# Kernel optimization log

Hardware: AMD Instinct MI355X
Metric: run time of the kernel (lower is better)

The kernel has to match this reference:

```python
import jax, jax.numpy as jnp
import numpy as np

N = 100000          # nodes
DEG = 32            # fixed in-degree (every node has a non-empty mailbox)
E = N * DEG         # edges
IN_DIM = 25         # node feature dim; 3 aggregators * 1 scaler * 25 = 75
OUT_DIM = 128
AGG_EPS = 1e-5      # PNA std aggregator epsilon
BN_EPS = 1e-5       # BatchNorm1d epsilon


def setup_inputs() -> dict:
    key = jax.random.key(0)
    k = jax.random.split(key, 6)
    h = jax.random.normal(k[0], (N, IN_DIM), dtype=jnp.float32)
    snorm_n = jax.random.uniform(k[1], (N, 1), dtype=jnp.float32)
    # every node appears exactly DEG times as a destination -> degree 32
    edge_dst = jnp.repeat(jnp.arange(N, dtype=jnp.int32), DEG)
    edge_src = jax.random.randint(k[2], (E,), 0, N, dtype=jnp.int32)
    # posttrans MLP (1 layer): Linear(75 -> 128), no final activation
    W = jax.random.normal(k[3], (3 * IN_DIM, OUT_DIM), dtype=jnp.float32) / np.sqrt(3 * IN_DIM)
    b = jnp.zeros((OUT_DIM,), dtype=jnp.float32)
    # BatchNorm1d affine params
    gamma = jnp.ones((OUT_DIM,), dtype=jnp.float32)
    beta = jnp.zeros((OUT_DIM,), dtype=jnp.float32)
    return {"h": h, "snorm_n": snorm_n, "edge_src": edge_src, "edge_dst": edge_dst,
            "W": W, "b": b, "gamma": gamma, "beta": beta}


def reference(h, snorm_n, edge_src, edge_dst, W, b, gamma, beta):
    # --- message: e = src node features (pretrans_edges + message_func) ---
    e = h[edge_src]                                   # [E, IN_DIM] irregular gather
    # --- reduce: mean / max / std over each destination's mailbox ---
    ones = jnp.ones((e.shape[0],), dtype=h.dtype)
    deg = jax.ops.segment_sum(ones, edge_dst, num_segments=N)
    deg = jnp.maximum(deg, 1.0)[:, None]              # [N, 1]
    s1 = jax.ops.segment_sum(e, edge_dst, num_segments=N)
    mean = s1 / deg                                   # aggregate_mean
    mx = jax.ops.segment_max(e, edge_dst, num_segments=N)  # aggregate_max
    s2 = jax.ops.segment_sum(e * e, edge_dst, num_segments=N)
    var = jax.nn.relu(s2 / deg - mean * mean)         # aggregate_var
    std = jnp.sqrt(var + AGG_EPS)                     # aggregate_std
    agg = jnp.concatenate([mean, mx, std], axis=1)    # [N, 75]; identity scaler only
    # --- posttrans MLP: single Linear(75 -> 128), last_activation='none' ---
    z = agg @ W + b                                   # [N, OUT_DIM]
    # --- graph norm ---
    z = z * snorm_n
    # --- BatchNorm1d (training mode: batch statistics, biased variance) ---
    mu = jnp.mean(z, axis=0)
    v = jnp.var(z, axis=0)
    z = (z - mu) / jnp.sqrt(v + BN_EPS) * gamma + beta
    # --- relu; residual disabled (in_dim != out_dim); dropout p=0.0 is no-op ---
    return jax.nn.relu(z)
```

## Files before the change

### kernel.cpp

```cpp
#include <hip/hip_runtime.h>
#include <hip/hip_bf16.h>

#define NN 100000
#define DEG 32
#define IN_DIM 25
#define AGG_DIM 75
#define KPAD 104
#define OUT_DIM 128
#define NPB 16
#define EPC (NPB * DEG)
#define NCHUNK (NN / NPB)
#define BLK 256
#define GRID 2048
#define PREP_GRID 391

typedef __attribute__((ext_vector_type(8))) short short8;
typedef __attribute__((ext_vector_type(4))) float f32x4;

static __device__ __forceinline__ unsigned f2bf(float x) {
    __hip_bfloat16 h = __float2bfloat16(x);
    return (unsigned)*reinterpret_cast<unsigned short*>(&h);
}
static __device__ __forceinline__ float bflo(unsigned v) { return __uint_as_float(v << 16); }
static __device__ __forceinline__ float bfhi(unsigned v) { return __uint_as_float(v & 0xffff0000u); }

static __device__ __forceinline__ void gload16(const void* g, void* l) {
    __builtin_amdgcn_global_load_lds(
        (const __attribute__((address_space(1))) unsigned*)g,
        (__attribute__((address_space(3))) unsigned*)l, 16, 0, 0);
}

__global__ __launch_bounds__(BLK) void prep(const float* __restrict__ h,
                                            ushort* __restrict__ hbp,
                                            float* __restrict__ bnbuf) {
    const int t = threadIdx.x;
    const int gid = blockIdx.x * BLK + t;
    if (gid < 2 * OUT_DIM) bnbuf[gid] = 0.0f;
    for (int n = gid; n < NN; n += PREP_GRID * BLK) {
        const float* row = h + n * IN_DIM;
        unsigned u[16];
        #pragma unroll
        for (int k = 0; k < 12; ++k) u[k] = f2bf(row[2 * k]) | (f2bf(row[2 * k + 1]) << 16);
        u[12] = f2bf(row[24]);
        u[13] = 0u; u[14] = 0u; u[15] = 0u;
        uint4* dst = (uint4*)(hbp + (size_t)n * 32);
        dst[0] = make_uint4(u[0], u[1], u[2], u[3]);
        dst[1] = make_uint4(u[4], u[5], u[6], u[7]);
        dst[2] = make_uint4(u[8], u[9], u[10], u[11]);
        dst[3] = make_uint4(u[12], u[13], u[14], u[15]);
    }
}

__global__ __launch_bounds__(BLK) void pna_main(
    const ushort* __restrict__ hb, const float* __restrict__ snorm,
    const int* __restrict__ esrc, const float* __restrict__ W,
    const float* __restrict__ b, float* __restrict__ z,
    float* __restrict__ bnbuf)
{
    __shared__ __align__(1024) ushort E_s[EPC][32];
    __shared__ int    ids_s[EPC];
    __shared__ ushort agg[NPB][KPAD];

    const int t = threadIdx.x;
    const int lane = t & 63;
    const int wv = t >> 6;

    for (int i = t; i < NPB * KPAD; i += BLK) ((ushort*)agg)[i] = 0;

    const int cb0 = (wv * 2 + 0) * 16 + (lane & 15);
    const int cb1 = (wv * 2 + 1) * 16 + (lane & 15);
    short8 bfrag[2][3];
    #pragma unroll
    for (int ct = 0; ct < 2; ++ct) {
        const int cb = ct ? cb1 : cb0;
        #pragma unroll
        for (int kt = 0; kt < 3; ++kt) {
            short8 fr;
            #pragma unroll
            for (int j = 0; j < 8; ++j) {
                const int k = kt * 32 + ((lane >> 4) * 8) + j;
                const float w = (k < AGG_DIM) ? W[k * OUT_DIM + cb] : 0.0f;
                fr[j] = (short)f2bf(w);
            }
            bfrag[ct][kt] = fr;
        }
    }
    const float bb0 = b[cb0], bb1 = b[cb1];

    const int lsub = lane >> 2;
    const int prt  = lane & 3;
    const int nl2 = t >> 4;
    const int f2  = t & 15;
    const bool a2act = (f2 < 13);
    const int dcol = f2 ^ ((nl2 & 3) << 2);

    float bns0 = 0.f, bnq0 = 0.f, bns1 = 0.f, bnq1 = 0.f;

    for (int chunk = blockIdx.x; chunk < NCHUNK; chunk += GRID) {
        const int n0 = chunk * NPB;

        ((int2*)ids_s)[t] = ((const int2*)(esrc + n0 * DEG))[t];
        __syncthreads();

        #pragma unroll
        for (int i = 0; i < 8; ++i) {
            const int g = wv * 8 + i;
            const int r = g * 16 + lsub;
            const int src = ids_s[r];
            const int psrc = prt ^ ((r >> 5) & 3);
            gload16((const char*)hb + ((size_t)src << 6) + (psrc << 4),
                    (char*)E_s + (g << 10));
        }
        __syncthreads();

        if (a2act) {
            const unsigned* Ew = (const unsigned*)E_s;
            const unsigned base = (unsigned)(nl2 * 512 + dcol);
            float s0 = 0.f, q0 = 0.f, m0 = -3.4e38f;
            float s1 = 0.f, q1 = 0.f, m1 = -3.4e38f;
            #pragma unroll
            for (int e = 0; e < 32; ++e) {
                const int ee = (e + nl2) & 31;
                const unsigned v = Ew[base + ee * 16];
                const float lo = bflo(v), hi = bfhi(v);
                s0 += lo; q0 = fmaf(lo, lo, q0); m0 = fmaxf(m0, lo);
                s1 += hi; q1 = fmaf(hi, hi, q1); m1 = fmaxf(m1, hi);
            }
            const float inv = 1.0f / DEG;
            const float mean0 = s0 * inv, var0 = fmaxf(q0 * inv - mean0 * mean0, 0.f);
            const float mean1 = s1 * inv, var1 = fmaxf(q1 * inv - mean1 * mean1, 0.f);
            const int ff = f2 * 2;
            agg[nl2][ff]              = (ushort)f2bf(mean0);
            agg[nl2][IN_DIM + ff]     = (ushort)f2bf(m0);
            agg[nl2][2 * IN_DIM + ff] = (ushort)f2bf(sqrtf(var0 + 1e-5f));
            if (ff + 1 < IN_DIM) {
                agg[nl2][ff + 1]              = (ushort)f2bf(mean1);
                agg[nl2][IN_DIM + ff + 1]     = (ushort)f2bf(m1);
                agg[nl2][2 * IN_DIM + ff + 1] = (ushort)f2bf(sqrtf(var1 + 1e-5f));
            }
        }
        __syncthreads();

        const int arow = lane & 15;
        const int ak0  = (lane >> 4) * 8;
        f32x4 acc0 = {0.f, 0.f, 0.f, 0.f}, acc1 = {0.f, 0.f, 0.f, 0.f};
        #pragma unroll
        for (int kt = 0; kt < 3; ++kt) {
            const short8 af = *reinterpret_cast<const short8*>(&agg[arow][kt * 32 + ak0]);
            acc0 = __builtin_amdgcn_mfma_f32_16x16x32_bf16(af, bfrag[0][kt], acc0, 0, 0, 0);
            acc1 = __builtin_amdgcn_mfma_f32_16x16x32_bf16(af, bfrag[1][kt], acc1, 0, 0, 0);
        }
        const int r0 = (lane >> 4) * 4;
        #pragma unroll
        for (int r = 0; r < 4; ++r) {
            const int node = n0 + r0 + r;
            const float sn = snorm[node];
            const float v0 = (acc0[r] + bb0) * sn;
            const float v1 = (acc1[r] + bb1) * sn;
            z[node * OUT_DIM + cb0] = v0;
            z[node * OUT_DIM + cb1] = v1;
            bns0 += v0; bnq0 = fmaf(v0, v0, bnq0);
            bns1 += v1; bnq1 = fmaf(v1, v1, bnq1);
        }
    }

    bns0 += __shfl_xor(bns0, 16); bnq0 += __shfl_xor(bnq0, 16);
    bns0 += __shfl_xor(bns0, 32); bnq0 += __shfl_xor(bnq0, 32);
    bns1 += __shfl_xor(bns1, 16); bnq1 += __shfl_xor(bnq1, 16);
    bns1 += __shfl_xor(bns1, 32); bnq1 += __shfl_xor(bnq1, 32);
    if ((lane >> 4) == 0) {
        atomicAdd(&bnbuf[cb0], bns0);
        atomicAdd(&bnbuf[OUT_DIM + cb0], bnq0);
        atomicAdd(&bnbuf[cb1], bns1);
        atomicAdd(&bnbuf[OUT_DIM + cb1], bnq1);
    }
}

__global__ __launch_bounds__(BLK) void bn_apply(
    const float* __restrict__ bnbuf, const float* __restrict__ gamma,
    const float* __restrict__ beta, float* __restrict__ z)
{
    __shared__ float sc_s[OUT_DIM], sh_s[OUT_DIM];
    const int t = threadIdx.x;
    if (t < OUT_DIM) {
        const float mu = bnbuf[t] * (1.0f / NN);
        const float v  = fmaxf(bnbuf[OUT_DIM + t] * (1.0f / NN) - mu * mu, 0.0f);
        const float sc = gamma[t] * rsqrtf(v + 1e-5f);
        sc_s[t] = sc;
        sh_s[t] = beta[t] - mu * sc;
    }
    __syncthreads();
    const int c4 = (t & 31) * 4;
    const float s0 = sc_s[c4], s1 = sc_s[c4+1], s2 = sc_s[c4+2], s3 = sc_s[c4+3];
    const float h0 = sh_s[c4], h1 = sh_s[c4+1], h2 = sh_s[c4+2], h3 = sh_s[c4+3];

    float4* z4 = (float4*)z;
    const int total4 = NN * (OUT_DIM / 4);
    for (int i = blockIdx.x * BLK + t; i < total4; i += gridDim.x * BLK) {
        float4 v = z4[i];
        v.x = fmaxf(fmaf(v.x, s0, h0), 0.f);
        v.y = fmaxf(fmaf(v.y, s1, h1), 0.f);
        v.z = fmaxf(fmaf(v.z, s2, h2), 0.f);
        v.w = fmaxf(fmaf(v.w, s3, h3), 0.f);
        z4[i] = v;
    }
}

extern "C" void kernel_launch(void* const* d_in, const int* in_sizes, int n_in,
                              void* d_out, int out_size, void* d_ws, size_t ws_size,
                              hipStream_t stream) {
    const float* h     = (const float*)d_in[0];
    const float* snorm = (const float*)d_in[1];
    const int*   esrc  = (const int*)d_in[2];
    const float* W     = (const float*)d_in[4];
    const float* b     = (const float*)d_in[5];
    const float* gamma = (const float*)d_in[6];
    const float* beta  = (const float*)d_in[7];
    float*  z     = (float*)d_out;
    float*  bnbuf = (float*)d_ws;
    ushort* hbp   = (ushort*)((char*)d_ws + 1024);

    prep<<<PREP_GRID, BLK, 0, stream>>>(h, hbp, bnbuf);
    pna_main<<<GRID, BLK, 0, stream>>>(hbp, snorm, esrc, W, b, z, bnbuf);
    bn_apply<<<2048, BLK, 0, stream>>>(bnbuf, gamma, beta, z);
}
```

Baseline: 186.2 us.

## Split gather into two feature-half passes staged in output buffer before matmul

The bf16 node table is split into two 32-byte halves (features 0-15 and 16-24), and the fused kernel is replaced by two gather/aggregate passes, one per half, plus a separate matmul kernel. Each pass writes its per-node aggregates into the output buffer as scratch, and the matmul kernel reads them back, reassembles the 75-wide row and applies the MFMA, snorm and BN statistics. The aim is to shrink each random gather's working set so the table fits better in cache, and to coalesce the prep kernel's reads through shared memory. The cost is two extra kernel launches, a second pass over the edge indices, and an extra global write and read of intermediate aggregates, which depends on the later z writes not overrunning slabs that have yet to be read.

```diff
diff --git a/kernel.cpp b/kernel.cpp
--- a/kernel.cpp
+++ b/kernel.cpp
@@ -5,14 +5,19 @@
 #define DEG 32
 #define IN_DIM 25
 #define AGG_DIM 75
+#define OUT_DIM 128
+#define BLK 256
+
+#define GNPB 32
+#define GEPC (GNPB * DEG)
+#define GGRID (NN / GNPB)
+
+#define MNPB 16
+#define MGRID 3125
 #define KPAD 104
-#define OUT_DIM 128
-#define NPB 16
-#define EPC (NPB * DEG)
-#define NCHUNK (NN / NPB)
-#define BLK 256
-#define GRID 2048
-#define PREP_GRID 391
+
+#define PREP_NPB 128
+#define PREP_GRID ((NN + PREP_NPB - 1) / PREP_NPB)
 
 typedef __attribute__((ext_vector_type(8))) short short8;
 typedef __attribute__((ext_vector_type(4))) float f32x4;
@@ -23,52 +28,128 @@
 }
 static __device__ __forceinline__ float bflo(unsigned v) { return __uint_as_float(v << 16); }
 static __device__ __forceinline__ float bfhi(unsigned v) { return __uint_as_float(v & 0xffff0000u); }
-
 static __device__ __forceinline__ void gload16(const void* g, void* l) {
     __builtin_amdgcn_global_load_lds(
         (const __attribute__((address_space(1))) unsigned*)g,
         (__attribute__((address_space(3))) unsigned*)l, 16, 0, 0);
 }
 
+
 __global__ __launch_bounds__(BLK) void prep(const float* __restrict__ h,
-                                            ushort* __restrict__ hbp,
+                                            ushort* __restrict__ tabA,
+                                            ushort* __restrict__ tabB,
                                             float* __restrict__ bnbuf) {
+    __shared__ float hls[PREP_NPB * IN_DIM];
+    const int t = threadIdx.x, bk = blockIdx.x;
+    if (bk == 0 && t < 2 * OUT_DIM) bnbuf[t] = 0.0f;
+    const int base4 = bk * (PREP_NPB * IN_DIM / 4);
+    const float4* h4 = (const float4*)h;
+    for (int i = t; i < PREP_NPB * IN_DIM / 4; i += BLK)
+        if (base4 + i < NN * IN_DIM / 4) ((float4*)hls)[i] = h4[base4 + i];
+    __syncthreads();
+    const int nl = t >> 1, sel = t & 1;
+    const int node = bk * PREP_NPB + nl;
+    if (node < NN) {
+        const float* row = hls + nl * IN_DIM;
+        unsigned u[8];
+        if (sel == 0) {
+            #pragma unroll
+            for (int k = 0; k < 8; ++k) u[k] = f2bf(row[2*k]) | (f2bf(row[2*k+1]) << 16);
+            uint4* d = (uint4*)(tabA + (size_t)node * 16);
+            d[0] = make_uint4(u[0],u[1],u[2],u[3]);
+            d[1] = make_uint4(u[4],u[5],u[6],u[7]);
+        } else {
+            #pragma unroll
+            for (int k = 0; k < 4; ++k) u[k] = f2bf(row[16+2*k]) | (f2bf(row[17+2*k]) << 16);
+            u[4] = f2bf(row[24]); u[5] = 0u; u[6] = 0u; u[7] = 0u;
+            uint4* d = (uint4*)(tabB + (size_t)node * 16);
+            d[0] = make_uint4(u[0],u[1],u[2],u[3]);
+            d[1] = make_uint4(u[4],u[5],u[6],u[7]);
+        }
+    }
+}
+
+template<int NF, int ODW, int OOFF>
+__global__ __launch_bounds__(BLK) void gather_pass(
+    const ushort* __restrict__ tab, const int* __restrict__ esrc,
+    unsigned* __restrict__ zdw)
+{
+    __shared__ __align__(1024) unsigned E_s[GEPC * 8];
+    __shared__ int ids_s[GEPC];
+    __shared__ unsigned aggT[GNPB * ODW];
+
     const int t = threadIdx.x;
-    const int gid = blockIdx.x * BLK + t;
-    if (gid < 2 * OUT_DIM) bnbuf[gid] = 0.0f;
-    for (int n = gid; n < NN; n += PREP_GRID * BLK) {
-        const float* row = h + n * IN_DIM;
-        unsigned u[16];
-        #pragma unroll
-        for (int k = 0; k < 12; ++k) u[k] = f2bf(row[2 * k]) | (f2bf(row[2 * k + 1]) << 16);
-        u[12] = f2bf(row[24]);
-        u[13] = 0u; u[14] = 0u; u[15] = 0u;
-        uint4* dst = (uint4*)(hbp + (size_t)n * 32);
-        dst[0] = make_uint4(u[0], u[1], u[2], u[3]);
-        dst[1] = make_uint4(u[4], u[5], u[6], u[7]);
-        dst[2] = make_uint4(u[8], u[9], u[10], u[11]);
-        dst[3] = make_uint4(u[12], u[13], u[14], u[15]);
-    }
-}
-
-__global__ __launch_bounds__(BLK) void pna_main(
-    const ushort* __restrict__ hb, const float* __restrict__ snorm,
-    const int* __restrict__ esrc, const float* __restrict__ W,
-    const float* __restrict__ b, float* __restrict__ z,
+    const int lane = t & 63, wv = t >> 6;
+    const int g0 = blockIdx.x;
+
+    ((int4*)ids_s)[t] = ((const int4*)(esrc + g0 * GEPC))[t];
+    __syncthreads();
+
+    const int lsub = lane >> 1, prt = lane & 1;
+    #pragma unroll
+    for (int i = 0; i < 8; ++i) {
+        const int g = wv * 8 + i;
+        const int src = ids_s[g * 32 + lsub];
+        gload16((const char*)tab + ((size_t)(unsigned)src << 5) + (prt << 4),
+                (char*)E_s + (g << 10));
+    }
+    __syncthreads();
+
+    const int nl = t >> 3, f = t & 7;
+    constexpr int SEC = (NF + 1) / 2;
+    if (f < SEC) {
+        const bool hasHi = (2 * f + 1 < NF);
+        float s0=0.f,q0=0.f,m0=-3.4e38f, s1=0.f,q1=0.f,m1=-3.4e38f;
+        const unsigned base = nl * 256 + f;
+        #pragma unroll
+        for (int e = 0; e < 32; ++e) {
+            const int ee = (e + nl) & 31;
+            const unsigned v = E_s[base + ee * 8];
+            const float lo = bflo(v), hi = bfhi(v);
+            s0 += lo; q0 = fmaf(lo,lo,q0); m0 = fmaxf(m0, lo);
+            s1 += hi; q1 = fmaf(hi,hi,q1); m1 = fmaxf(m1, hi);
+        }
+        const float inv = 1.0f / DEG;
+        const float mean0 = s0*inv, var0 = fmaxf(q0*inv - mean0*mean0, 0.f);
+        const float mean1 = s1*inv, var1 = fmaxf(q1*inv - mean1*mean1, 0.f);
+        unsigned dmean = f2bf(mean0), dmax = f2bf(m0), dstd = f2bf(sqrtf(var0+1e-5f));
+        if (hasHi) {
+            dmean |= f2bf(mean1) << 16;
+            dmax  |= f2bf(m1)    << 16;
+            dstd  |= f2bf(sqrtf(var1+1e-5f)) << 16;
+        }
+        aggT[nl*ODW + f]         = dmean;
+        aggT[nl*ODW + SEC + f]   = dmax;
+        aggT[nl*ODW + 2*SEC + f] = dstd;
+    } else if (NF == 9 && f == 5) {
+        aggT[nl*ODW + 15] = 0u;
+    }
+    __syncthreads();
+
+    constexpr int HALF = (GNPB/2) * ODW;
+    for (int i = t; i < GNPB * ODW; i += BLK) {
+        const int s = i / HALF, j = i - s * HALF;
+        __builtin_nontemporal_store(aggT[i],
+            zdw + (size_t)(2*g0 + s) * 2048 + OOFF + j);
+    }
+}
+
+__global__ __launch_bounds__(BLK) void mm(
+    const float* __restrict__ snorm, const float* __restrict__ W,
+    const float* __restrict__ bias, float* __restrict__ z,
     float* __restrict__ bnbuf)
 {
-    __shared__ __align__(1024) ushort E_s[EPC][32];
-    __shared__ int    ids_s[EPC];
-    __shared__ ushort agg[NPB][KPAD];
+    __shared__ ushort sA[MNPB * 48];
+    __shared__ ushort sB[MNPB * 32];
+    __shared__ ushort tile[MNPB * KPAD];
 
     const int t = threadIdx.x;
-    const int lane = t & 63;
-    const int wv = t >> 6;
-
-    for (int i = t; i < NPB * KPAD; i += BLK) ((ushort*)agg)[i] = 0;
-
-    const int cb0 = (wv * 2 + 0) * 16 + (lane & 15);
-    const int cb1 = (wv * 2 + 1) * 16 + (lane & 15);
+    const int lane = t & 63, wv = t >> 6;
+
+    for (int i = t; i < MNPB * KPAD; i += BLK) tile[i] = 0;
+
+    const int cb0 = (wv*2+0)*16 + (lane & 15);
+    const int cb1 = (wv*2+1)*16 + (lane & 15);
     short8 bfrag[2][3];
     #pragma unroll
     for (int ct = 0; ct < 2; ++ct) {
@@ -78,96 +159,68 @@
             short8 fr;
             #pragma unroll
             for (int j = 0; j < 8; ++j) {
-                const int k = kt * 32 + ((lane >> 4) * 8) + j;
+                const int k = kt*32 + (lane>>4)*8 + j;
                 const float w = (k < AGG_DIM) ? W[k * OUT_DIM + cb] : 0.0f;
                 fr[j] = (short)f2bf(w);
             }
             bfrag[ct][kt] = fr;
         }
     }
-    const float bb0 = b[cb0], bb1 = b[cb1];
-
-    const int lsub = lane >> 2;
-    const int prt  = lane & 3;
-    const int nl2 = t >> 4;
-    const int f2  = t & 15;
-    const bool a2act = (f2 < 13);
-    const int dcol = f2 ^ ((nl2 & 3) << 2);
-
-    float bns0 = 0.f, bnq0 = 0.f, bns1 = 0.f, bnq1 = 0.f;
-
-    for (int chunk = blockIdx.x; chunk < NCHUNK; chunk += GRID) {
-        const int n0 = chunk * NPB;
-
-        ((int2*)ids_s)[t] = ((const int2*)(esrc + n0 * DEG))[t];
+    const float bb0 = bias[cb0], bb1 = bias[cb1];
+
+    float bns0=0.f,bnq0=0.f,bns1=0.f,bnq1=0.f;
+    const unsigned* zdw = (const unsigned*)z;
+
+    for (int c = 0; c < 2; ++c) {
+        const int chunk = blockIdx.x * 2 + c;
+        const int n0 = chunk * MNPB;
+        const unsigned* slab = zdw + (size_t)chunk * 2048;
+        for (int i = t; i < 384; i += BLK) ((unsigned*)sA)[i] = slab[i];
+        ((unsigned*)sB)[t] = slab[384 + t];
         __syncthreads();
-
-        #pragma unroll
-        for (int i = 0; i < 8; ++i) {
-            const int g = wv * 8 + i;
-            const int r = g * 16 + lsub;
-            const int src = ids_s[r];
-            const int psrc = prt ^ ((r >> 5) & 3);
-            gload16((const char*)hb + ((size_t)src << 6) + (psrc << 4),
-                    (char*)E_s + (g << 10));
+        {
+            const int n = t & 15;
+            const ushort* rA = sA + n*48;
+            const ushort* rB = sB + n*32;
+            for (int k = t >> 4; k < AGG_DIM; k += 16) {
+                ushort v;
+                if      (k < 16) v = rA[k];
+                else if (k < 25) v = rB[k-16];
+                else if (k < 41) v = rA[k-9];
+                else if (k < 50) v = rB[k-31];
+                else if (k < 66) v = rA[k-18];
+                else             v = rB[k-46];
+                tile[n*KPAD + k] = v;
+            }
         }
         __syncthreads();
-
-        if (a2act) {
-            const unsigned* Ew = (const unsigned*)E_s;
-            const unsigned base = (unsigned)(nl2 * 512 + dcol);
-            float s0 = 0.f, q0 = 0.f, m0 = -3.4e38f;
-            float s1 = 0.f, q1 = 0.f, m1 = -3.4e38f;
-            #pragma unroll
-            for (int e = 0; e < 32; ++e) {
-                const int ee = (e + nl2) & 31;
-                const unsigned v = Ew[base + ee * 16];
-                const float lo = bflo(v), hi = bfhi(v);
-                s0 += lo; q0 = fmaf(lo, lo, q0); m0 = fmaxf(m0, lo);
-                s1 += hi; q1 = fmaf(hi, hi, q1); m1 = fmaxf(m1, hi);
-            }
-            const float inv = 1.0f / DEG;
-            const float mean0 = s0 * inv, var0 = fmaxf(q0 * inv - mean0 * mean0, 0.f);
-            const float mean1 = s1 * inv, var1 = fmaxf(q1 * inv - mean1 * mean1, 0.f);
-            const int ff = f2 * 2;
-            agg[nl2][ff]              = (ushort)f2bf(mean0);
-            agg[nl2][IN_DIM + ff]     = (ushort)f2bf(m0);
-            agg[nl2][2 * IN_DIM + ff] = (ushort)f2bf(sqrtf(var0 + 1e-5f));
-            if (ff + 1 < IN_DIM) {
-                agg[nl2][ff + 1]              = (ushort)f2bf(mean1);
-                agg[nl2][IN_DIM + ff + 1]     = (ushort)f2bf(m1);
-                agg[nl2][2 * IN_DIM + ff + 1] = (ushort)f2bf(sqrtf(var1 + 1e-5f));
-            }
-        }
-        __syncthreads();
-
-        const int arow = lane & 15;
-        const int ak0  = (lane >> 4) * 8;
-        f32x4 acc0 = {0.f, 0.f, 0.f, 0.f}, acc1 = {0.f, 0.f, 0.f, 0.f};
+        const int arow = lane & 15, ak0 = (lane>>4)*8;
+        f32x4 acc0 = {0.f,0.f,0.f,0.f}, acc1 = {0.f,0.f,0.f,0.f};
         #pragma unroll
         for (int kt = 0; kt < 3; ++kt) {
-            const short8 af = *reinterpret_cast<const short8*>(&agg[arow][kt * 32 + ak0]);
-            acc0 = __builtin_amdgcn_mfma_f32_16x16x32_bf16(af, bfrag[0][kt], acc0, 0, 0, 0);
-            acc1 = __builtin_amdgcn_mfma_f32_16x16x32_bf16(af, bfrag[1][kt], acc1, 0, 0, 0);
-        }
-        const int r0 = (lane >> 4) * 4;
+            const short8 af = *(const short8*)(tile + arow*KPAD + kt*32 + ak0);
+            acc0 = __builtin_amdgcn_mfma_f32_16x16x32_bf16(af, bfrag[0][kt], acc0, 0,0,0);
+            acc1 = __builtin_amdgcn_mfma_f32_16x16x32_bf16(af, bfrag[1][kt], acc1, 0,0,0);
+        }
+        const int r0 = (lane>>4)*4;
         #pragma unroll
         for (int r = 0; r < 4; ++r) {
             const int node = n0 + r0 + r;
             const float sn = snorm[node];
             const float v0 = (acc0[r] + bb0) * sn;
             const float v1 = (acc1[r] + bb1) * sn;
-            z[node * OUT_DIM + cb0] = v0;
-            z[node * OUT_DIM + cb1] = v1;
-            bns0 += v0; bnq0 = fmaf(v0, v0, bnq0);
-            bns1 += v1; bnq1 = fmaf(v1, v1, bnq1);
-        }
-    }
-
-    bns0 += __shfl_xor(bns0, 16); bnq0 += __shfl_xor(bnq0, 16);
-    bns0 += __shfl_xor(bns0, 32); bnq0 += __shfl_xor(bnq0, 32);
-    bns1 += __shfl_xor(bns1, 16); bnq1 += __shfl_xor(bnq1, 16);
-    bns1 += __shfl_xor(bns1, 32); bnq1 += __shfl_xor(bnq1, 32);
+            z[node*OUT_DIM + cb0] = v0;
+            z[node*OUT_DIM + cb1] = v1;
+            bns0 += v0; bnq0 = fmaf(v0,v0,bnq0);
+            bns1 += v1; bnq1 = fmaf(v1,v1,bnq1);
+        }
+        __syncthreads();
+    }
+
+    bns0 += __shfl_xor(bns0,16); bnq0 += __shfl_xor(bnq0,16);
+    bns0 += __shfl_xor(bns0,32); bnq0 += __shfl_xor(bnq0,32);
+    bns1 += __shfl_xor(bns1,16); bnq1 += __shfl_xor(bnq1,16);
+    bns1 += __shfl_xor(bns1,32); bnq1 += __shfl_xor(bnq1,32);
     if ((lane >> 4) == 0) {
         atomicAdd(&bnbuf[cb0], bns0);
         atomicAdd(&bnbuf[OUT_DIM + cb0], bnq0);
@@ -218,9 +271,12 @@
     const float* beta  = (const float*)d_in[7];
     float*  z     = (float*)d_out;
     float*  bnbuf = (float*)d_ws;
-    ushort* hbp   = (ushort*)((char*)d_ws + 1024);
-
-    prep<<<PREP_GRID, BLK, 0, stream>>>(h, hbp, bnbuf);
-    pna_main<<<GRID, BLK, 0, stream>>>(hbp, snorm, esrc, W, b, z, bnbuf);
+    ushort* tabA  = (ushort*)((char*)d_ws + 1024);
+    ushort* tabB  = (ushort*)((char*)d_ws + 1024 + (size_t)NN * 32);
+
+    prep<<<PREP_GRID, BLK, 0, stream>>>(h, tabA, tabB, bnbuf);
+    gather_pass<16, 24, 0  ><<<GGRID, BLK, 0, stream>>>(tabA, esrc, (unsigned*)d_out);
+    gather_pass< 9, 16, 384><<<GGRID, BLK, 0, stream>>>(tabB, esrc, (unsigned*)d_out);
+    mm<<<MGRID, BLK, 0, stream>>>(snorm, W, b, z, bnbuf);
     bn_apply<<<2048, BLK, 0, stream>>>(bnbuf, gamma, beta, z);
 }
```

New measurement: 240.5 us. +29.2%, slower.
